# Performance work log

Measured on AMD Instinct MI355X. Metric: run time of the kernel, lower is better.

Reference implementation:

```python
import jax, jax.numpy as jnp
import numpy as np

HEADS = 4
W1 = 7
W2 = 5

def _ln_channel(x, g, b):
    # x: [B,C,H,W]; LayerNorm over channel dim (permute to channel-last)
    xt = x.transpose(0, 2, 3, 1)
    mu = xt.mean(-1, keepdims=True)
    var = xt.var(-1, keepdims=True)
    xt = (xt - mu) / jnp.sqrt(var + 1e-5) * g + b
    return xt.transpose(0, 3, 1, 2)

def _neighborhood_attention(x, qkv_w, qkv_b, proj_w, proj_b, rpb, heads, w):
    # x: [B,C,H,W]; clamped sliding-window (NAT) attention with rel-pos bias
    B, C, H, Wd = x.shape
    hd = C // heads
    xl = x.transpose(0, 2, 3, 1)                      # [B,H,W,C]
    qkv = xl @ qkv_w.T + qkv_b                        # [B,H,W,3C]
    qkv = qkv.reshape(B, H, Wd, 3, heads, hd)
    q = qkv[:, :, :, 0].transpose(0, 3, 1, 2, 4)      # [B,h,H,W,d]
    k = qkv[:, :, :, 1].transpose(0, 3, 1, 2, 4)
    v = qkv[:, :, :, 2].transpose(0, 3, 1, 2, 4)
    q = q * (hd ** -0.5)
    # clamped neighborhood start per row/col
    si = jnp.clip(jnp.arange(H) - w // 2, 0, H - w)   # [H]
    sj = jnp.clip(jnp.arange(Wd) - w // 2, 0, Wd - w) # [W]
    idx_i = si[:, None] + jnp.arange(w)[None, :]      # [H,w]
    idx_j = sj[:, None] + jnp.arange(w)[None, :]      # [W,w]
    # gather neighbor keys/values: [B,h,H,W,w,w,d]
    k_nb = k[:, :, idx_i[:, None, :, None], idx_j[None, :, None, :], :]
    v_nb = v[:, :, idx_i[:, None, :, None], idx_j[None, :, None, :], :]
    attn = jnp.einsum('bnijd,bnijkld->bnijkl', q, k_nb)  # [B,h,H,W,w,w]
    # relative position bias: rel = (w-1) + neighbor_offset - query_offset
    pi = jnp.arange(H) - si                            # [H] in [0,w-1]
    pj = jnp.arange(Wd) - sj
    bi = (w - 1) + jnp.arange(w)[None, :] - pi[:, None]  # [H,w]
    bj = (w - 1) + jnp.arange(w)[None, :] - pj[:, None]  # [W,w]
    bias = rpb[:, bi[:, None, :, None], bj[None, :, None, :]]  # [h,H,W,w,w]
    attn = attn + bias[None]
    attn = jax.nn.softmax(attn.reshape(B, heads, H, Wd, w * w), axis=-1)
    attn = attn.reshape(B, heads, H, Wd, w, w)
    out = jnp.einsum('bnijkl,bnijkld->bnijd', attn, v_nb)  # [B,h,H,W,d]
    out = out.transpose(0, 2, 3, 1, 4).reshape(B, H, Wd, C)
    out = out @ proj_w.T + proj_b
    return out.transpose(0, 3, 1, 2)                   # [B,C,H,W]

def setup_inputs() -> dict:
    key = jax.random.key(0)
    ks = jax.random.split(key, 12)
    B, C, H, W = 2, 128, 56, 56
    s = 0.02
    return {
        'x': jax.random.normal(ks[0], (B, C, H, W), jnp.float32),
        'ln1_g': jnp.ones((C,), jnp.float32),
        'ln1_b': jnp.zeros((C,), jnp.float32),
        'qkv_w1': jax.random.normal(ks[1], (3 * C, C), jnp.float32) * s,
        'qkv_b1': jnp.zeros((3 * C,), jnp.float32),
        'proj_w1': jax.random.normal(ks[2], (C, C), jnp.float32) * s,
        'proj_b1': jnp.zeros((C,), jnp.float32),
        'rpb1': jax.random.normal(ks[3], (HEADS, 2 * W1 - 1, 2 * W1 - 1), jnp.float32) * s,
        'qkv_w2': jax.random.normal(ks[4], (3 * C, C), jnp.float32) * s,
        'qkv_b2': jnp.zeros((3 * C,), jnp.float32),
        'proj_w2': jax.random.normal(ks[5], (C, C), jnp.float32) * s,
        'proj_b2': jnp.zeros((C,), jnp.float32),
        'rpb2': jax.random.normal(ks[6], (HEADS, 2 * W2 - 1, 2 * W2 - 1), jnp.float32) * s,
        'ln2_g': jnp.ones((C,), jnp.float32),
        'ln2_b': jnp.zeros((C,), jnp.float32),
        'fc1_w': jax.random.normal(ks[7], (2 * C, C), jnp.float32) * s,
        'fc1_b': jnp.zeros((2 * C,), jnp.float32),
        'fc2_w': jax.random.normal(ks[8], (C, 2 * C), jnp.float32) * s,
        'fc2_b': jnp.zeros((C,), jnp.float32),
    }

def reference(x, ln1_g, ln1_b, qkv_w1, qkv_b1, proj_w1, proj_b1, rpb1,
              qkv_w2, qkv_b2, proj_w2, proj_b2, rpb2,
              ln2_g, ln2_b, fc1_w, fc1_b, fc2_w, fc2_b):
    xn = _ln_channel(x, ln1_g, ln1_b)
    a = (_neighborhood_attention(xn, qkv_w1, qkv_b1, proj_w1, proj_b1, rpb1, HEADS, W1)
         + _neighborhood_attention(xn, qkv_w2, qkv_b2, proj_w2, proj_b2, rpb2, HEADS, W2))
    x = x + a
    xn2 = _ln_channel(x, ln2_g, ln2_b)
    h = jnp.einsum('bchw,oc->bohw', xn2, fc1_w) + fc1_b[None, :, None, None]
    h = jax.nn.gelu(h, approximate=False)  # torch nn.GELU default = exact erf
    y = jnp.einsum('bchw,oc->bohw', h, fc2_w) + fc2_b[None, :, None, None]
    return x + y
```

## Files before the change

kernel.cpp:

```cpp
#include <hip/hip_runtime.h>
#include <hip/hip_bf16.h>

#define BATCH 2
#define CH    128
#define HH    56
#define WW    56
#define HWS   3136
#define NPOS  6272
#define HEADS 4
#define HD    32

using f32x4 = __attribute__((ext_vector_type(4))) float;
using s16x8 = __attribute__((ext_vector_type(8))) short;

__device__ __forceinline__ unsigned short f2bf(float f) {
  unsigned u = __builtin_bit_cast(unsigned, f);
  u += 0x7FFFu + ((u >> 16) & 1u);
  return (unsigned short)(u >> 16);
}
__device__ __forceinline__ unsigned pack2bf(float a, float b) {
  return (unsigned)f2bf(a) | ((unsigned)f2bf(b) << 16);
}
__device__ __forceinline__ float4 bf4tof(uint2 u) {
  float4 r;
  r.x = __builtin_bit_cast(float, u.x << 16);
  r.y = __builtin_bit_cast(float, u.x & 0xFFFF0000u);
  r.z = __builtin_bit_cast(float, u.y << 16);
  r.w = __builtin_bit_cast(float, u.y & 0xFFFF0000u);
  return r;
}

__global__ __launch_bounds__(256) void convert_weights(
    const float* __restrict__ qw1, const float* __restrict__ qw2,
    const float* __restrict__ pw1, const float* __restrict__ pw2,
    const float* __restrict__ f1w, const float* __restrict__ f2w,
    unsigned short* __restrict__ wb) {
  int bid = blockIdx.x;
  const float* src; unsigned short* dst; int base;
  if (bid < 48)       { src = qw1; dst = wb;           base = bid * 1024; }
  else if (bid < 96)  { src = qw2; dst = wb + 49152;   base = (bid - 48) * 1024; }
  else if (bid < 112) { src = pw1; dst = wb + 98304;   base = (bid - 96) * 1024; }
  else if (bid < 128) { src = pw2; dst = wb + 114688;  base = (bid - 112) * 1024; }
  else if (bid < 160) { src = f1w; dst = wb + 131072;  base = (bid - 128) * 1024; }
  else                { src = f2w; dst = wb + 163840;  base = (bid - 160) * 1024; }
  int i = base + threadIdx.x * 4;
  float4 v = *reinterpret_cast<const float4*>(src + i);
  uint2 o;
  o.x = pack2bf(v.x, v.y);
  o.y = pack2bf(v.z, v.w);
  *reinterpret_cast<uint2*>(dst + i) = o;
}

__global__ __launch_bounds__(256) void ln1_kernel(const float* __restrict__ x,
                                                  const float* __restrict__ g,
                                                  const float* __restrict__ be,
                                                  unsigned short* __restrict__ out) {
  __shared__ float tile[128 * 65];
  __shared__ float mu_s[64];
  __shared__ float rs_s[64];
  const int p0 = blockIdx.x * 64;
  const int b  = (p0 >= HWS) ? 1 : 0;
  const int s0 = p0 - b * HWS;
  const int tid = threadIdx.x;

  for (int idx = tid; idx < 8192; idx += 256) {
    int c = idx >> 6, p = idx & 63;
    tile[c * 65 + p] = x[(size_t)(b * CH + c) * HWS + s0 + p];
  }
  __syncthreads();
  {
    int p = tid >> 2, q = tid & 3;
    float sum = 0.f, sq = 0.f;
#pragma unroll
    for (int t = 0; t < 32; ++t) {
      float v = tile[(q * 32 + t) * 65 + p];
      sum += v; sq += v * v;
    }
    sum += __shfl_xor(sum, 1); sq += __shfl_xor(sq, 1);
    sum += __shfl_xor(sum, 2); sq += __shfl_xor(sq, 2);
    float mu  = sum * 0.0078125f;
    float var = sq * 0.0078125f - mu * mu;
    float rs  = rsqrtf(var + 1e-5f);
    if (q == 0) { mu_s[p] = mu; rs_s[p] = rs; }
  }
  __syncthreads();
  for (int idx = tid; idx < 4096; idx += 256) {
    int nl = idx >> 6, c2 = idx & 63;
    int c0 = 2 * c2;
    float v0 = (tile[c0 * 65 + nl] - mu_s[nl]) * rs_s[nl] * g[c0] + be[c0];
    float v1 = (tile[(c0 + 1) * 65 + nl] - mu_s[nl]) * rs_s[nl] * g[c0 + 1] + be[c0 + 1];
    reinterpret_cast<unsigned*>(out)[(size_t)(p0 + nl) * 64 + c2] = pack2bf(v0, v1);
  }
}

__device__ __forceinline__ void stage64(const unsigned short* __restrict__ src,
                                        int stride, int row0, int kc,
                                        int tid, char* dstB) {
#pragma unroll
  for (int c = 0; c < 2; ++c) {
    int lin = c * 256 + tid;
    int row = lin >> 3;
    int k8  = (lin & 7) << 3;
    int byte = (row << 7) + (k8 << 1);
    byte ^= (row & 7) << 4;
    *reinterpret_cast<uint4*>(dstB + byte) =
        *reinterpret_cast<const uint4*>(src + (size_t)(row0 + row) * stride + kc + k8);
  }
}

__device__ __forceinline__ void tile_compute(const char* AsB, int aStrideB, int aKoffB,
                                             const char* WsB, int lane, int wr, int wc,
                                             f32x4 (&acc)[2][2]) {
  const int r_lo = lane & 15, kg = lane >> 4;
#pragma unroll
  for (int ks = 0; ks < 2; ++ks) {
    const int koffW = ks * 64 + kg * 16;
    const int koffA = aKoffB + koffW;
    s16x8 a[2], bf[2];
#pragma unroll
    for (int fi = 0; fi < 2; ++fi) {
      int row = wr * 32 + fi * 16 + r_lo;
      int byte = row * aStrideB + koffA; byte ^= (row & 7) << 4;
      a[fi] = *reinterpret_cast<const s16x8*>(AsB + byte);
    }
#pragma unroll
    for (int ci = 0; ci < 2; ++ci) {
      int row = wc * 32 + ci * 16 + r_lo;
      int byte = (row << 7) + koffW; byte ^= (row & 7) << 4;
      bf[ci] = *reinterpret_cast<const s16x8*>(WsB + byte);
    }
#pragma unroll
    for (int fi = 0; fi < 2; ++fi)
#pragma unroll
      for (int ci = 0; ci < 2; ++ci)
        acc[fi][ci] = __builtin_amdgcn_mfma_f32_16x16x32_bf16(a[fi], bf[ci], acc[fi][ci], 0, 0, 0);
  }
}

__device__ __forceinline__ float gelu_exact(float v) {
  return 0.5f * v * (1.0f + erff(v * 0.70710678118654752f));
}

__global__ __launch_bounds__(256) void qkv_mfma(const unsigned short* __restrict__ A,
                                                const unsigned short* __restrict__ W1,
                                                const float* __restrict__ b1,
                                                unsigned short* __restrict__ o1,
                                                const unsigned short* __restrict__ W2,
                                                const float* __restrict__ b2,
                                                unsigned short* __restrict__ o2) {
  __shared__ char AsB[8192];
  __shared__ char WsB[8192];
  const int tid = threadIdx.x;
  const int lane = tid & 63, w = tid >> 6, wr = w >> 1, wc = w & 1;
  const int p0 = blockIdx.x * 64;
  const int yy = blockIdx.y;
  const bool first = yy < 6;
  const unsigned short* W = first ? W1 : W2;
  const float* bias = first ? b1 : b2;
  unsigned short* outp = first ? o1 : o2;
  const int n0 = (first ? yy : yy - 6) * 64;

  f32x4 acc[2][2];
#pragma unroll
  for (int i = 0; i < 2; ++i)
#pragma unroll
    for (int j = 0; j < 2; ++j) acc[i][j] = (f32x4){0.f, 0.f, 0.f, 0.f};

  for (int kc = 0; kc < 128; kc += 64) {
    if (kc) __syncthreads();
    stage64(A, 128, p0, kc, tid, AsB);
    stage64(W, 128, n0, kc, tid, WsB);
    __syncthreads();
    tile_compute(AsB, 128, 0, WsB, lane, wr, wc, acc);
  }
  const int r_lo = lane & 15, kg = lane >> 4;
#pragma unroll
  for (int ci = 0; ci < 2; ++ci) {
    int col = n0 + wc * 32 + ci * 16 + r_lo;
    float bc = bias[col];
#pragma unroll
    for (int fi = 0; fi < 2; ++fi) {
      int row0 = p0 + wr * 32 + fi * 16 + kg * 4;
#pragma unroll
      for (int r = 0; r < 4; ++r)
        outp[(size_t)(row0 + r) * 384 + col] = f2bf(acc[fi][ci][r] + bc);
    }
  }
}

__global__ __launch_bounds__(256) void proj_mfma(const unsigned short* __restrict__ A1,
                                                 const unsigned short* __restrict__ W1,
                                                 const float* __restrict__ b1,
                                                 const unsigned short* __restrict__ A2,
                                                 const unsigned short* __restrict__ W2,
                                                 const float* __restrict__ b2,
                                                 const float* __restrict__ xres,
                                                 float* __restrict__ x2out) {
  __shared__ char AsB[8192];
  __shared__ char WsB[8192];
  const int tid = threadIdx.x;
  const int lane = tid & 63, w = tid >> 6, wr = w >> 1, wc = w & 1;
  const int p0 = blockIdx.x * 64, n0 = blockIdx.y * 64;
  const int bb = (p0 >= HWS) ? 1 : 0;
  const int s0 = p0 - bb * HWS;
  f32x4 acc[2][2];
#pragma unroll
  for (int i = 0; i < 2; ++i)
#pragma unroll
    for (int j = 0; j < 2; ++j) acc[i][j] = (f32x4){0.f, 0.f, 0.f, 0.f};

  const unsigned short* Ap[2] = {A1, A2};
  const unsigned short* Wp[2] = {W1, W2};
#pragma unroll
  for (int s2 = 0; s2 < 2; ++s2) {
    for (int kc = 0; kc < 128; kc += 64) {
      if (s2 || kc) __syncthreads();
      stage64(Ap[s2], 128, p0, kc, tid, AsB);
      stage64(Wp[s2], 128, n0, kc, tid, WsB);
      __syncthreads();
      tile_compute(AsB, 128, 0, WsB, lane, wr, wc, acc);
    }
  }
  const int r_lo = lane & 15, kg = lane >> 4;
#pragma unroll
  for (int ci = 0; ci < 2; ++ci) {
    int col = n0 + wc * 32 + ci * 16 + r_lo;
    float bc = b1[col] + b2[col];
#pragma unroll
    for (int fi = 0; fi < 2; ++fi) {
      int rloc = wr * 32 + fi * 16 + kg * 4;
      float4 xr = *reinterpret_cast<const float4*>(
          &xres[(size_t)(bb * CH + col) * HWS + s0 + rloc]);
      int row0 = p0 + rloc;
      x2out[(size_t)(row0 + 0) * CH + col] = acc[fi][ci][0] + bc + xr.x;
      x2out[(size_t)(row0 + 1) * CH + col] = acc[fi][ci][1] + bc + xr.y;
      x2out[(size_t)(row0 + 2) * CH + col] = acc[fi][ci][2] + bc + xr.z;
      x2out[(size_t)(row0 + 3) * CH + col] = acc[fi][ci][3] + bc + xr.w;
    }
  }
}

__global__ __launch_bounds__(256) void fc1ln_mfma(const float* __restrict__ x2,
                                                  const float* __restrict__ g,
                                                  const float* __restrict__ be,
                                                  const unsigned short* __restrict__ W,
                                                  const float* __restrict__ bias,
                                                  unsigned short* __restrict__ out) {
  __shared__ char AsB[16384];
  __shared__ char WsB[8192];
  const int tid = threadIdx.x;
  const int lane = tid & 63, w = tid >> 6, wr = w >> 1, wc = w & 1;
  const int p0 = blockIdx.x * 64, n0 = blockIdx.y * 64;
  {
    const int p = tid >> 2, q = tid & 3;
    const float* row = x2 + (size_t)(p0 + p) * CH + q * 32;
    float4 v[8];
    float sum = 0.f, sq = 0.f;
#pragma unroll
    for (int t = 0; t < 8; ++t) {
      v[t] = *reinterpret_cast<const float4*>(row + t * 4);
      sum += v[t].x + v[t].y + v[t].z + v[t].w;
      sq  += v[t].x * v[t].x + v[t].y * v[t].y + v[t].z * v[t].z + v[t].w * v[t].w;
    }
    sum += __shfl_xor(sum, 1); sq += __shfl_xor(sq, 1);
    sum += __shfl_xor(sum, 2); sq += __shfl_xor(sq, 2);
    float mu = sum * 0.0078125f;
    float rs = rsqrtf(sq * 0.0078125f - mu * mu + 1e-5f);
#pragma unroll
    for (int t = 0; t < 8; t += 2) {
      int d0 = q * 32 + t * 4;
      float4 g0 = *reinterpret_cast<const float4*>(g + d0);
      float4 g1 = *reinterpret_cast<const float4*>(g + d0 + 4);
      float4 b0 = *reinterpret_cast<const float4*>(be + d0);
      float4 b1v = *reinterpret_cast<const float4*>(be + d0 + 4);
      uint4 o;
      o.x = pack2bf((v[t].x - mu) * rs * g0.x + b0.x, (v[t].y - mu) * rs * g0.y + b0.y);
      o.y = pack2bf((v[t].z - mu) * rs * g0.z + b0.z, (v[t].w - mu) * rs * g0.w + b0.w);
      o.z = pack2bf((v[t+1].x - mu) * rs * g1.x + b1v.x, (v[t+1].y - mu) * rs * g1.y + b1v.y);
      o.w = pack2bf((v[t+1].z - mu) * rs * g1.z + b1v.z, (v[t+1].w - mu) * rs * g1.w + b1v.w);
      int byte = p * 256 + q * 64 + (t >> 1) * 16;
      byte ^= (p & 7) << 4;
      *reinterpret_cast<uint4*>(AsB + byte) = o;
    }
  }
  f32x4 acc[2][2];
#pragma unroll
  for (int i = 0; i < 2; ++i)
#pragma unroll
    for (int j = 0; j < 2; ++j) acc[i][j] = (f32x4){0.f, 0.f, 0.f, 0.f};

  for (int kc = 0; kc < 128; kc += 64) {
    __syncthreads();
    stage64(W, 128, n0, kc, tid, WsB);
    __syncthreads();
    tile_compute(AsB, 256, kc * 2, WsB, lane, wr, wc, acc);
  }
  const int r_lo = lane & 15, kg = lane >> 4;
#pragma unroll
  for (int ci = 0; ci < 2; ++ci) {
    int col = n0 + wc * 32 + ci * 16 + r_lo;
    float bc = bias[col];
#pragma unroll
    for (int fi = 0; fi < 2; ++fi) {
      int row0 = p0 + wr * 32 + fi * 16 + kg * 4;
#pragma unroll
      for (int r = 0; r < 4; ++r)
        out[(size_t)(row0 + r) * 256 + col] = f2bf(gelu_exact(acc[fi][ci][r] + bc));
    }
  }
}

__global__ __launch_bounds__(256) void fc2_mfma(const unsigned short* __restrict__ A,
                                                const unsigned short* __restrict__ W,
                                                const float* __restrict__ bias,
                                                const float* __restrict__ x2,
                                                float* __restrict__ out) {
  __shared__ char AsB[8192];
  __shared__ char WsB[8192];
  const int tid = threadIdx.x;
  const int lane = tid & 63, w = tid >> 6, wr = w >> 1, wc = w & 1;
  const int p0 = blockIdx.x * 64, n0 = blockIdx.y * 64;
  const int bb = (p0 >= HWS) ? 1 : 0;
  const int s0 = p0 - bb * HWS;
  f32x4 acc[2][2];
#pragma unroll
  for (int i = 0; i < 2; ++i)
#pragma unroll
    for (int j = 0; j < 2; ++j) acc[i][j] = (f32x4){0.f, 0.f, 0.f, 0.f};

  for (int kc = 0; kc < 256; kc += 64) {
    if (kc) __syncthreads();
    stage64(A, 256, p0, kc, tid, AsB);
    stage64(W, 256, n0, kc, tid, WsB);
    __syncthreads();
    tile_compute(AsB, 128, 0, WsB, lane, wr, wc, acc);
  }
  const int r_lo = lane & 15, kg = lane >> 4;
#pragma unroll
  for (int ci = 0; ci < 2; ++ci) {
    int col = n0 + wc * 32 + ci * 16 + r_lo;
    float bc = bias[col];
#pragma unroll
    for (int fi = 0; fi < 2; ++fi) {
      int rloc = wr * 32 + fi * 16 + kg * 4;
      int row0 = p0 + rloc;
      float4 o;
      o.x = acc[fi][ci][0] + bc + x2[(size_t)(row0 + 0) * CH + col];
      o.y = acc[fi][ci][1] + bc + x2[(size_t)(row0 + 1) * CH + col];
      o.z = acc[fi][ci][2] + bc + x2[(size_t)(row0 + 2) * CH + col];
      o.w = acc[fi][ci][3] + bc + x2[(size_t)(row0 + 3) * CH + col];
      *reinterpret_cast<float4*>(&out[(size_t)(bb * CH + col) * HWS + s0 + rloc]) = o;
    }
  }
}

template <int NW>
__device__ __forceinline__ void natten_body(const unsigned short* __restrict__ qkvb,
                                            const float* __restrict__ rpb,
                                            unsigned short* __restrict__ out,
                                            int blk, int tid) {
  const int g   = blk * 32 + (tid >> 3);
  const int sub = tid & 7;
  const int j  = g % WW;
  const int t1 = g / WW;
  const int i  = t1 % HH;
  const int t2 = t1 / HH;
  const int h  = t2 & 3;
  const int b  = t2 >> 2;
  const int n  = b * HWS + i * WW + j;

  const float scale = 0.17677669529663687f;
  float4 q = bf4tof(*reinterpret_cast<const uint2*>(qkvb + (size_t)n * 384 + h * 32 + sub * 4));
  q.x *= scale; q.y *= scale; q.z *= scale; q.w *= scale;

  const int si = min(max(i - NW / 2, 0), HH - NW);
  const int sj = min(max(j - NW / 2, 0), WW - NW);
  const float* rb = rpb + h * (2 * NW - 1) * (2 * NW - 1)
                    + (NW - 1 - (i - si)) * (2 * NW - 1) + (NW - 1 - (j - sj));
  float sc[NW * NW];
  float mx = -1e30f;
#pragma unroll
  for (int ki = 0; ki < NW; ++ki) {
#pragma unroll
    for (int kj = 0; kj < NW; ++kj) {
      const int nn = b * HWS + (si + ki) * WW + sj + kj;
      float4 k4 = bf4tof(*reinterpret_cast<const uint2*>(
          qkvb + (size_t)nn * 384 + 128 + h * 32 + sub * 4));
      float p = q.x * k4.x + q.y * k4.y + q.z * k4.z + q.w * k4.w;
      p += __shfl_xor(p, 1);
      p += __shfl_xor(p, 2);
      p += __shfl_xor(p, 4);
      p += rb[ki * (2 * NW - 1) + kj];
      sc[ki * NW + kj] = p;
      mx = fmaxf(mx, p);
    }
  }
  float ssum = 0.f;
#pragma unroll
  for (int kk = 0; kk < NW * NW; ++kk) {
    sc[kk] = __expf(sc[kk] - mx);
    ssum += sc[kk];
  }
  float4 o = make_float4(0.f, 0.f, 0.f, 0.f);
#pragma unroll
  for (int ki = 0; ki < NW; ++ki) {
#pragma unroll
    for (int kj = 0; kj < NW; ++kj) {
      const int nn = b * HWS + (si + ki) * WW + sj + kj;
      float4 v4 = bf4tof(*reinterpret_cast<const uint2*>(
          qkvb + (size_t)nn * 384 + 256 + h * 32 + sub * 4));
      float p = sc[ki * NW + kj];
      o.x = fmaf(p, v4.x, o.x);
      o.y = fmaf(p, v4.y, o.y);
      o.z = fmaf(p, v4.z, o.z);
      o.w = fmaf(p, v4.w, o.w);
    }
  }
  float inv = 1.0f / ssum;
  uint2 ov;
  ov.x = pack2bf(o.x * inv, o.y * inv);
  ov.y = pack2bf(o.z * inv, o.w * inv);
  *reinterpret_cast<uint2*>(out + (size_t)n * CH + h * 32 + sub * 4) = ov;
}

__global__ __launch_bounds__(256) void natten_fused(const unsigned short* __restrict__ qkv1,
                                                    const float* __restrict__ rpb1,
                                                    unsigned short* __restrict__ a1,
                                                    const unsigned short* __restrict__ qkv2,
                                                    const float* __restrict__ rpb2,
                                                    unsigned short* __restrict__ a2) {
  if (blockIdx.x < 784) natten_body<7>(qkv1, rpb1, a1, blockIdx.x, threadIdx.x);
  else                  natten_body<5>(qkv2, rpb2, a2, blockIdx.x - 784, threadIdx.x);
}

extern "C" void kernel_launch(void* const* d_in, const int* in_sizes, int n_in,
                              void* d_out, int out_size, void* d_ws, size_t ws_size,
                              hipStream_t stream) {
  const float* x       = (const float*)d_in[0];
  const float* ln1_g   = (const float*)d_in[1];
  const float* ln1_b   = (const float*)d_in[2];
  const float* qkv_w1  = (const float*)d_in[3];
  const float* qkv_b1  = (const float*)d_in[4];
  const float* proj_w1 = (const float*)d_in[5];
  const float* proj_b1 = (const float*)d_in[6];
  const float* rpb1    = (const float*)d_in[7];
  const float* qkv_w2  = (const float*)d_in[8];
  const float* qkv_b2  = (const float*)d_in[9];
  const float* proj_w2 = (const float*)d_in[10];
  const float* proj_b2 = (const float*)d_in[11];
  const float* rpb2    = (const float*)d_in[12];
  const float* ln2_g   = (const float*)d_in[13];
  const float* ln2_b   = (const float*)d_in[14];
  const float* fc1_w   = (const float*)d_in[15];
  const float* fc1_b   = (const float*)d_in[16];
  const float* fc2_w   = (const float*)d_in[17];
  const float* fc2_b   = (const float*)d_in[18];
  float* out = (float*)d_out;

  char* wsb = (char*)d_ws;
  unsigned short* xn    = (unsigned short*)(wsb);
  unsigned short* qkv1  = (unsigned short*)(wsb + 1605632);
  unsigned short* qkv2  = (unsigned short*)(wsb + 6422528);
  unsigned short* attn1 = (unsigned short*)(wsb + 11239424);
  unsigned short* attn2 = (unsigned short*)(wsb + 12845056);
  float*          x2    = (float*)(wsb + 14450688);
  unsigned short* hbuf  = (unsigned short*)(wsb + 17661952);
  unsigned short* wbuf  = (unsigned short*)(wsb + 20873216);

  unsigned short* qw1b = wbuf;
  unsigned short* qw2b = wbuf + 49152;
  unsigned short* pw1b = wbuf + 98304;
  unsigned short* pw2b = wbuf + 114688;
  unsigned short* f1wb = wbuf + 131072;
  unsigned short* f2wb = wbuf + 163840;

  convert_weights<<<192, 256, 0, stream>>>(qkv_w1, qkv_w2, proj_w1, proj_w2,
                                           fc1_w, fc2_w, wbuf);
  ln1_kernel<<<98, 256, 0, stream>>>(x, ln1_g, ln1_b, xn);
  qkv_mfma<<<dim3(98, 12), 256, 0, stream>>>(xn, qw1b, qkv_b1, qkv1, qw2b, qkv_b2, qkv2);
  natten_fused<<<1568, 256, 0, stream>>>(qkv1, rpb1, attn1, qkv2, rpb2, attn2);
  proj_mfma<<<dim3(98, 2), 256, 0, stream>>>(attn1, pw1b, proj_b1,
                                             attn2, pw2b, proj_b2, x, x2);
  fc1ln_mfma<<<dim3(98, 4), 256, 0, stream>>>(x2, ln2_g, ln2_b, f1wb, fc1_b, hbuf);
  fc2_mfma<<<dim3(98, 2), 256, 0, stream>>>(hbuf, f2wb, fc2_b, x2, out);
}
```

Measured before the change: 156.3 us.

## Fuse LN1 into QKV GEMM, convert weights inline, stage NATTEN K/V rows in LDS

After: 183.2 us. 1.17x slower.

```diff
diff --git a/kernel.cpp b/kernel.cpp
--- a/kernel.cpp
+++ b/kernel.cpp
@@ -30,69 +30,6 @@
   return r;
 }
 
-__global__ __launch_bounds__(256) void convert_weights(
-    const float* __restrict__ qw1, const float* __restrict__ qw2,
-    const float* __restrict__ pw1, const float* __restrict__ pw2,
-    const float* __restrict__ f1w, const float* __restrict__ f2w,
-    unsigned short* __restrict__ wb) {
-  int bid = blockIdx.x;
-  const float* src; unsigned short* dst; int base;
-  if (bid < 48)       { src = qw1; dst = wb;           base = bid * 1024; }
-  else if (bid < 96)  { src = qw2; dst = wb + 49152;   base = (bid - 48) * 1024; }
-  else if (bid < 112) { src = pw1; dst = wb + 98304;   base = (bid - 96) * 1024; }
-  else if (bid < 128) { src = pw2; dst = wb + 114688;  base = (bid - 112) * 1024; }
-  else if (bid < 160) { src = f1w; dst = wb + 131072;  base = (bid - 128) * 1024; }
-  else                { src = f2w; dst = wb + 163840;  base = (bid - 160) * 1024; }
-  int i = base + threadIdx.x * 4;
-  float4 v = *reinterpret_cast<const float4*>(src + i);
-  uint2 o;
-  o.x = pack2bf(v.x, v.y);
-  o.y = pack2bf(v.z, v.w);
-  *reinterpret_cast<uint2*>(dst + i) = o;
-}
-
-__global__ __launch_bounds__(256) void ln1_kernel(const float* __restrict__ x,
-                                                  const float* __restrict__ g,
-                                                  const float* __restrict__ be,
-                                                  unsigned short* __restrict__ out) {
-  __shared__ float tile[128 * 65];
-  __shared__ float mu_s[64];
-  __shared__ float rs_s[64];
-  const int p0 = blockIdx.x * 64;
-  const int b  = (p0 >= HWS) ? 1 : 0;
-  const int s0 = p0 - b * HWS;
-  const int tid = threadIdx.x;
-
-  for (int idx = tid; idx < 8192; idx += 256) {
-    int c = idx >> 6, p = idx & 63;
-    tile[c * 65 + p] = x[(size_t)(b * CH + c) * HWS + s0 + p];
-  }
-  __syncthreads();
-  {
-    int p = tid >> 2, q = tid & 3;
-    float sum = 0.f, sq = 0.f;
-#pragma unroll
-    for (int t = 0; t < 32; ++t) {
-      float v = tile[(q * 32 + t) * 65 + p];
-      sum += v; sq += v * v;
-    }
-    sum += __shfl_xor(sum, 1); sq += __shfl_xor(sq, 1);
-    sum += __shfl_xor(sum, 2); sq += __shfl_xor(sq, 2);
-    float mu  = sum * 0.0078125f;
-    float var = sq * 0.0078125f - mu * mu;
-    float rs  = rsqrtf(var + 1e-5f);
-    if (q == 0) { mu_s[p] = mu; rs_s[p] = rs; }
-  }
-  __syncthreads();
-  for (int idx = tid; idx < 4096; idx += 256) {
-    int nl = idx >> 6, c2 = idx & 63;
-    int c0 = 2 * c2;
-    float v0 = (tile[c0 * 65 + nl] - mu_s[nl]) * rs_s[nl] * g[c0] + be[c0];
-    float v1 = (tile[(c0 + 1) * 65 + nl] - mu_s[nl]) * rs_s[nl] * g[c0 + 1] + be[c0 + 1];
-    reinterpret_cast<unsigned*>(out)[(size_t)(p0 + nl) * 64 + c2] = pack2bf(v0, v1);
-  }
-}
-
 __device__ __forceinline__ void stage64(const unsigned short* __restrict__ src,
                                         int stride, int row0, int kc,
                                         int tid, char* dstB) {
@@ -108,6 +45,28 @@
   }
 }
 
+__device__ __forceinline__ void stage64_f32(const float* __restrict__ src,
+                                            int stride, int row0, int kc,
+                                            int tid, char* dstB) {
+#pragma unroll
+  for (int c = 0; c < 2; ++c) {
+    int lin = c * 256 + tid;
+    int row = lin >> 3;
+    int k8  = (lin & 7) << 3;
+    int byte = (row << 7) + (k8 << 1);
+    byte ^= (row & 7) << 4;
+    const float* s = src + (size_t)(row0 + row) * stride + kc + k8;
+    float4 va = *reinterpret_cast<const float4*>(s);
+    float4 vb = *reinterpret_cast<const float4*>(s + 4);
+    uint4 o;
+    o.x = pack2bf(va.x, va.y);
+    o.y = pack2bf(va.z, va.w);
+    o.z = pack2bf(vb.x, vb.y);
+    o.w = pack2bf(vb.z, vb.w);
+    *reinterpret_cast<uint4*>(dstB + byte) = o;
+  }
+}
+
 __device__ __forceinline__ void tile_compute(const char* AsB, int aStrideB, int aKoffB,
                                              const char* WsB, int lane, int wr, int wc,
                                              f32x4 (&acc)[2][2]) {
@@ -141,25 +100,63 @@
   return 0.5f * v * (1.0f + erff(v * 0.70710678118654752f));
 }
 
-__global__ __launch_bounds__(256) void qkv_mfma(const unsigned short* __restrict__ A,
-                                                const unsigned short* __restrict__ W1,
-                                                const float* __restrict__ b1,
-                                                unsigned short* __restrict__ o1,
-                                                const unsigned short* __restrict__ W2,
-                                                const float* __restrict__ b2,
-                                                unsigned short* __restrict__ o2) {
-  __shared__ char AsB[8192];
+__global__ __launch_bounds__(256) void qkv_ln1_mfma(const float* __restrict__ x,
+                                                    const float* __restrict__ g,
+                                                    const float* __restrict__ be,
+                                                    const float* __restrict__ W1f,
+                                                    const float* __restrict__ b1,
+                                                    unsigned short* __restrict__ o1,
+                                                    const float* __restrict__ W2f,
+                                                    const float* __restrict__ b2,
+                                                    unsigned short* __restrict__ o2) {
+  __shared__ float tileF[128 * 65];
+  __shared__ float mu_s[64];
+  __shared__ float rs_s[64];
+  __shared__ char AsB[16384];
   __shared__ char WsB[8192];
   const int tid = threadIdx.x;
   const int lane = tid & 63, w = tid >> 6, wr = w >> 1, wc = w & 1;
   const int p0 = blockIdx.x * 64;
+  const int bb = (p0 >= HWS) ? 1 : 0;
+  const int s0 = p0 - bb * HWS;
   const int yy = blockIdx.y;
   const bool first = yy < 6;
-  const unsigned short* W = first ? W1 : W2;
+  const float* Wf = first ? W1f : W2f;
   const float* bias = first ? b1 : b2;
   unsigned short* outp = first ? o1 : o2;
   const int n0 = (first ? yy : yy - 6) * 64;
 
+  for (int idx = tid; idx < 8192; idx += 256) {
+    int c = idx >> 6, p = idx & 63;
+    tileF[c * 65 + p] = x[(size_t)(bb * CH + c) * HWS + s0 + p];
+  }
+  __syncthreads();
+  {
+    int p = tid >> 2, q = tid & 3;
+    float sum = 0.f, sq = 0.f;
+#pragma unroll
+    for (int t = 0; t < 32; ++t) {
+      float v = tileF[(q * 32 + t) * 65 + p];
+      sum += v; sq += v * v;
+    }
+    sum += __shfl_xor(sum, 1); sq += __shfl_xor(sq, 1);
+    sum += __shfl_xor(sum, 2); sq += __shfl_xor(sq, 2);
+    float mu  = sum * 0.0078125f;
+    float var = sq * 0.0078125f - mu * mu;
+    float rs  = rsqrtf(var + 1e-5f);
+    if (q == 0) { mu_s[p] = mu; rs_s[p] = rs; }
+  }
+  __syncthreads();
+  for (int idx = tid; idx < 4096; idx += 256) {
+    int nl = idx >> 6, c2 = idx & 63;
+    int c0 = 2 * c2;
+    float v0 = (tileF[c0 * 65 + nl] - mu_s[nl]) * rs_s[nl] * g[c0] + be[c0];
+    float v1 = (tileF[(c0 + 1) * 65 + nl] - mu_s[nl]) * rs_s[nl] * g[c0 + 1] + be[c0 + 1];
+    int byte = nl * 256 + c0 * 2;
+    byte ^= (nl & 7) << 4;
+    *reinterpret_cast<unsigned*>(AsB + byte) = pack2bf(v0, v1);
+  }
+
   f32x4 acc[2][2];
 #pragma unroll
   for (int i = 0; i < 2; ++i)
@@ -167,11 +164,10 @@
     for (int j = 0; j < 2; ++j) acc[i][j] = (f32x4){0.f, 0.f, 0.f, 0.f};
 
   for (int kc = 0; kc < 128; kc += 64) {
-    if (kc) __syncthreads();
-    stage64(A, 128, p0, kc, tid, AsB);
-    stage64(W, 128, n0, kc, tid, WsB);
     __syncthreads();
-    tile_compute(AsB, 128, 0, WsB, lane, wr, wc, acc);
+    stage64_f32(Wf, 128, n0, kc, tid, WsB);
+    __syncthreads();
+    tile_compute(AsB, 256, kc * 2, WsB, lane, wr, wc, acc);
   }
   const int r_lo = lane & 15, kg = lane >> 4;
 #pragma unroll
@@ -189,10 +185,10 @@
 }
 
 __global__ __launch_bounds__(256) void proj_mfma(const unsigned short* __restrict__ A1,
-                                                 const unsigned short* __restrict__ W1,
+                                                 const float* __restrict__ W1f,
                                                  const float* __restrict__ b1,
                                                  const unsigned short* __restrict__ A2,
-                                                 const unsigned short* __restrict__ W2,
+                                                 const float* __restrict__ W2f,
                                                  const float* __restrict__ b2,
                                                  const float* __restrict__ xres,
                                                  float* __restrict__ x2out) {
@@ -210,13 +206,13 @@
     for (int j = 0; j < 2; ++j) acc[i][j] = (f32x4){0.f, 0.f, 0.f, 0.f};
 
   const unsigned short* Ap[2] = {A1, A2};
-  const unsigned short* Wp[2] = {W1, W2};
+  const float* Wp[2] = {W1f, W2f};
 #pragma unroll
   for (int s2 = 0; s2 < 2; ++s2) {
     for (int kc = 0; kc < 128; kc += 64) {
       if (s2 || kc) __syncthreads();
       stage64(Ap[s2], 128, p0, kc, tid, AsB);
-      stage64(Wp[s2], 128, n0, kc, tid, WsB);
+      stage64_f32(Wp[s2], 128, n0, kc, tid, WsB);
       __syncthreads();
       tile_compute(AsB, 128, 0, WsB, lane, wr, wc, acc);
     }
@@ -243,7 +239,7 @@
 __global__ __launch_bounds__(256) void fc1ln_mfma(const float* __restrict__ x2,
                                                   const float* __restrict__ g,
                                                   const float* __restrict__ be,
-                                                  const unsigned short* __restrict__ W,
+                                                  const float* __restrict__ Wf,
                                                   const float* __restrict__ bias,
                                                   unsigned short* __restrict__ out) {
   __shared__ char AsB[16384];
@@ -291,7 +287,7 @@
 
   for (int kc = 0; kc < 128; kc += 64) {
     __syncthreads();
-    stage64(W, 128, n0, kc, tid, WsB);
+    stage64_f32(Wf, 128, n0, kc, tid, WsB);
     __syncthreads();
     tile_compute(AsB, 256, kc * 2, WsB, lane, wr, wc, acc);
   }
@@ -311,7 +307,7 @@
 }
 
 __global__ __launch_bounds__(256) void fc2_mfma(const unsigned short* __restrict__ A,
-                                                const unsigned short* __restrict__ W,
+                                                const float* __restrict__ Wf,
                                                 const float* __restrict__ bias,
                                                 const float* __restrict__ x2,
                                                 float* __restrict__ out) {
@@ -331,7 +327,7 @@
   for (int kc = 0; kc < 256; kc += 64) {
     if (kc) __syncthreads();
     stage64(A, 256, p0, kc, tid, AsB);
-    stage64(W, 256, n0, kc, tid, WsB);
+    stage64_f32(Wf, 256, n0, kc, tid, WsB);
     __syncthreads();
     tile_compute(AsB, 128, 0, WsB, lane, wr, wc, acc);
   }
@@ -355,82 +351,100 @@
 }
 
 template <int NW>
-__device__ __forceinline__ void natten_body(const unsigned short* __restrict__ qkvb,
-                                            const float* __restrict__ rpb,
-                                            unsigned short* __restrict__ out,
-                                            int blk, int tid) {
-  const int g   = blk * 32 + (tid >> 3);
-  const int sub = tid & 7;
-  const int j  = g % WW;
-  const int t1 = g / WW;
-  const int i  = t1 % HH;
-  const int t2 = t1 / HH;
+__device__ __forceinline__ void natten_lds_body(const unsigned short* __restrict__ qkvb,
+                                                const float* __restrict__ rpb,
+                                                unsigned short* __restrict__ out,
+                                                int blk, int tid,
+                                                unsigned short* Ks, unsigned short* Vs) {
+  const int i  = blk % HH;
+  const int t2 = blk / HH;
   const int h  = t2 & 3;
   const int b  = t2 >> 2;
-  const int n  = b * HWS + i * WW + j;
-
+  const int si = min(max(i - NW / 2, 0), HH - NW);
+
+  const int nparts = NW * 56 * 4;
+  for (int u0 = 0; u0 < nparts; u0 += 256) {
+    int lin = u0 + tid;
+    if (lin < nparts) {
+      int unit = lin >> 2, part = lin & 3;
+      int r = unit / 56, c = unit % 56;
+      const unsigned short* gk =
+          qkvb + (size_t)(b * HWS + (si + r) * WW + c) * 384 + 128 + h * 32 + part * 8;
+      *reinterpret_cast<uint4*>(reinterpret_cast<char*>(Ks) + lin * 16) =
+          *reinterpret_cast<const uint4*>(gk);
+      *reinterpret_cast<uint4*>(reinterpret_cast<char*>(Vs) + lin * 16) =
+          *reinterpret_cast<const uint4*>(gk + 128);
+    }
+  }
+  __syncthreads();
+
+  const int grp = tid >> 3, sub = tid & 7;
   const float scale = 0.17677669529663687f;
-  float4 q = bf4tof(*reinterpret_cast<const uint2*>(qkvb + (size_t)n * 384 + h * 32 + sub * 4));
-  q.x *= scale; q.y *= scale; q.z *= scale; q.w *= scale;
-
-  const int si = min(max(i - NW / 2, 0), HH - NW);
-  const int sj = min(max(j - NW / 2, 0), WW - NW);
-  const float* rb = rpb + h * (2 * NW - 1) * (2 * NW - 1)
-                    + (NW - 1 - (i - si)) * (2 * NW - 1) + (NW - 1 - (j - sj));
-  float sc[NW * NW];
-  float mx = -1e30f;
-#pragma unroll
-  for (int ki = 0; ki < NW; ++ki) {
-#pragma unroll
-    for (int kj = 0; kj < NW; ++kj) {
-      const int nn = b * HWS + (si + ki) * WW + sj + kj;
-      float4 k4 = bf4tof(*reinterpret_cast<const uint2*>(
-          qkvb + (size_t)nn * 384 + 128 + h * 32 + sub * 4));
-      float p = q.x * k4.x + q.y * k4.y + q.z * k4.z + q.w * k4.w;
-      p += __shfl_xor(p, 1);
-      p += __shfl_xor(p, 2);
-      p += __shfl_xor(p, 4);
-      p += rb[ki * (2 * NW - 1) + kj];
-      sc[ki * NW + kj] = p;
-      mx = fmaxf(mx, p);
-    }
-  }
-  float ssum = 0.f;
-#pragma unroll
-  for (int kk = 0; kk < NW * NW; ++kk) {
-    sc[kk] = __expf(sc[kk] - mx);
-    ssum += sc[kk];
-  }
-  float4 o = make_float4(0.f, 0.f, 0.f, 0.f);
-#pragma unroll
-  for (int ki = 0; ki < NW; ++ki) {
-#pragma unroll
-    for (int kj = 0; kj < NW; ++kj) {
-      const int nn = b * HWS + (si + ki) * WW + sj + kj;
-      float4 v4 = bf4tof(*reinterpret_cast<const uint2*>(
-          qkvb + (size_t)nn * 384 + 256 + h * 32 + sub * 4));
-      float p = sc[ki * NW + kj];
-      o.x = fmaf(p, v4.x, o.x);
-      o.y = fmaf(p, v4.y, o.y);
-      o.z = fmaf(p, v4.z, o.z);
-      o.w = fmaf(p, v4.w, o.w);
-    }
-  }
-  float inv = 1.0f / ssum;
-  uint2 ov;
-  ov.x = pack2bf(o.x * inv, o.y * inv);
-  ov.y = pack2bf(o.z * inv, o.w * inv);
-  *reinterpret_cast<uint2*>(out + (size_t)n * CH + h * 32 + sub * 4) = ov;
-}
-
-__global__ __launch_bounds__(256) void natten_fused(const unsigned short* __restrict__ qkv1,
-                                                    const float* __restrict__ rpb1,
-                                                    unsigned short* __restrict__ a1,
-                                                    const unsigned short* __restrict__ qkv2,
-                                                    const float* __restrict__ rpb2,
-                                                    unsigned short* __restrict__ a2) {
-  if (blockIdx.x < 784) natten_body<7>(qkv1, rpb1, a1, blockIdx.x, threadIdx.x);
-  else                  natten_body<5>(qkv2, rpb2, a2, blockIdx.x - 784, threadIdx.x);
+  for (int j = grp; j < WW; j += 32) {
+    const int n = b * HWS + i * WW + j;
+    float4 q = bf4tof(*reinterpret_cast<const uint2*>(
+        qkvb + (size_t)n * 384 + h * 32 + sub * 4));
+    q.x *= scale; q.y *= scale; q.z *= scale; q.w *= scale;
+
+    const int sj = min(max(j - NW / 2, 0), WW - NW);
+    const float* rb = rpb + h * (2 * NW - 1) * (2 * NW - 1)
+                      + (NW - 1 - (i - si)) * (2 * NW - 1) + (NW - 1 - (j - sj));
+    float sc[NW * NW];
+    float mx = -1e30f;
+#pragma unroll
+    for (int ki = 0; ki < NW; ++ki) {
+#pragma unroll
+      for (int kj = 0; kj < NW; ++kj) {
+        const unsigned short* kp = Ks + ((ki * 56) + sj + kj) * 32 + sub * 4;
+        float4 k4 = bf4tof(*reinterpret_cast<const uint2*>(kp));
+        float p = q.x * k4.x + q.y * k4.y + q.z * k4.z + q.w * k4.w;
+        p += __shfl_xor(p, 1);
+        p += __shfl_xor(p, 2);
+        p += __shfl_xor(p, 4);
+        p += rb[ki * (2 * NW - 1) + kj];
+        sc[ki * NW + kj] = p;
+        mx = fmaxf(mx, p);
+      }
+    }
+    float ssum = 0.f;
+#pragma unroll
+    for (int kk = 0; kk < NW * NW; ++kk) {
+      sc[kk] = __expf(sc[kk] - mx);
+      ssum += sc[kk];
+    }
+    float4 o = make_float4(0.f, 0.f, 0.f, 0.f);
+#pragma unroll
+    for (int ki = 0; ki < NW; ++ki) {
+#pragma unroll
+      for (int kj = 0; kj < NW; ++kj) {
+        const unsigned short* vp = Vs + ((ki * 56) + sj + kj) * 32 + sub * 4;
+        float4 v4 = bf4tof(*reinterpret_cast<const uint2*>(vp));
+        float p = sc[ki * NW + kj];
+        o.x = fmaf(p, v4.x, o.x);
+        o.y = fmaf(p, v4.y, o.y);
+        o.z = fmaf(p, v4.z, o.z);
+        o.w = fmaf(p, v4.w, o.w);
+      }
+    }
+    float inv = 1.0f / ssum;
+    uint2 ov;
+    ov.x = pack2bf(o.x * inv, o.y * inv);
+    ov.y = pack2bf(o.z * inv, o.w * inv);
+    *reinterpret_cast<uint2*>(out + (size_t)n * CH + h * 32 + sub * 4) = ov;
+  }
+}
+
+__global__ __launch_bounds__(256) void natten_both(const unsigned short* __restrict__ qkv1,
+                                                   const float* __restrict__ rpb1,
+                                                   unsigned short* __restrict__ a1,
+                                                   const unsigned short* __restrict__ qkv2,
+                                                   const float* __restrict__ rpb2,
+                                                   unsigned short* __restrict__ a2) {
+  __shared__ unsigned short kv[2 * 7 * 56 * 32];
+  if (blockIdx.x < 448)
+    natten_lds_body<7>(qkv1, rpb1, a1, blockIdx.x, threadIdx.x, kv, kv + 7 * 56 * 32);
+  else
+    natten_lds_body<5>(qkv2, rpb2, a2, blockIdx.x - 448, threadIdx.x, kv, kv + 7 * 56 * 32);
 }
 
 extern "C" void kernel_launch(void* const* d_in, const int* in_sizes, int n_in,
@@ -458,29 +472,19 @@
   float* out = (float*)d_out;
 
   char* wsb = (char*)d_ws;
-  unsigned short* xn    = (unsigned short*)(wsb);
-  unsigned short* qkv1  = (unsigned short*)(wsb + 1605632);
-  unsigned short* qkv2  = (unsigned short*)(wsb + 6422528);
-  unsigned short* attn1 = (unsigned short*)(wsb + 11239424);
-  unsigned short* attn2 = (unsigned short*)(wsb + 12845056);
-  float*          x2    = (float*)(wsb + 14450688);
-  unsigned short* hbuf  = (unsigned short*)(wsb + 17661952);
-  unsigned short* wbuf  = (unsigned short*)(wsb + 20873216);
-
-  unsigned short* qw1b = wbuf;
-  unsigned short* qw2b = wbuf + 49152;
-  unsigned short* pw1b = wbuf + 98304;
-  unsigned short* pw2b = wbuf + 114688;
-  unsigned short* f1wb = wbuf + 131072;
-  unsigned short* f2wb = wbuf + 163840;
-
-  convert_weights<<<192, 256, 0, stream>>>(qkv_w1, qkv_w2, proj_w1, proj_w2,
-                                           fc1_w, fc2_w, wbuf);
-  ln1_kernel<<<98, 256, 0, stream>>>(x, ln1_g, ln1_b, xn);
-  qkv_mfma<<<dim3(98, 12), 256, 0, stream>>>(xn, qw1b, qkv_b1, qkv1, qw2b, qkv_b2, qkv2);
-  natten_fused<<<1568, 256, 0, stream>>>(qkv1, rpb1, attn1, qkv2, rpb2, attn2);
-  proj_mfma<<<dim3(98, 2), 256, 0, stream>>>(attn1, pw1b, proj_b1,
-                                             attn2, pw2b, proj_b2, x, x2);
-  fc1ln_mfma<<<dim3(98, 4), 256, 0, stream>>>(x2, ln2_g, ln2_b, f1wb, fc1_b, hbuf);
-  fc2_mfma<<<dim3(98, 2), 256, 0, stream>>>(hbuf, f2wb, fc2_b, x2, out);
-}
+  unsigned short* qkv1  = (unsigned short*)(wsb);
+  unsigned short* qkv2  = (unsigned short*)(wsb + 4816896);
+  unsigned short* attn1 = (unsigned short*)(wsb + 9633792);
+  unsigned short* attn2 = (unsigned short*)(wsb + 11239424);
+  float*          x2    = (float*)(wsb + 12845056);
+  unsigned short* hbuf  = (unsigned short*)(wsb + 16056320);
+
+  qkv_ln1_mfma<<<dim3(98, 12), 256, 0, stream>>>(x, ln1_g, ln1_b,
+                                                 qkv_w1, qkv_b1, qkv1,
+                                                 qkv_w2, qkv_b2, qkv2);
+  natten_both<<<896, 256, 0, stream>>>(qkv1, rpb1, attn1, qkv2, rpb2, attn2);
+  proj_mfma<<<dim3(98, 2), 256, 0, stream>>>(attn1, proj_w1, proj_b1,
+                                             attn2, proj_w2, proj_b2, x, x2);
+  fc1ln_mfma<<<dim3(98, 4), 256, 0, stream>>>(x2, ln2_g, ln2_b, fc1_w, fc1_b, hbuf);
+  fc2_mfma<<<dim3(98, 2), 256, 0, stream>>>(hbuf, fc2_w, fc2_b, x2, out);
+}
```
